# Optimization experiments

Measured on AMD Instinct MI355X. Metric: run time of the kernel, lower is better.

Reference implementation:

```python
import jax, jax.numpy as jnp
import numpy as np
import math

H = 32       # num_attention_heads
HKV = 8      # num_key_value_heads
D = 128      # attention_head_size


def setup_inputs() -> dict:
    key = jax.random.key(0)
    k1, k2, k3 = jax.random.split(key, 3)
    B, L = 2, 2048
    return {
        "query_states": jax.random.normal(k1, (B, L, H * D), dtype=jnp.float32),
        "key_states": jax.random.normal(k2, (B, L, HKV * D), dtype=jnp.float32),
        "value_states": jax.random.normal(k3, (B, L, HKV * D), dtype=jnp.float32),
    }


def reference(query_states, key_states, value_states):
    B, L, _ = query_states.shape
    groups = H // HKV

    # view + transpose(1,2): (B, heads, L, D)
    q = query_states.reshape(B, L, H, D).transpose(0, 2, 1, 3)
    k = key_states.reshape(B, L, HKV, D).transpose(0, 2, 1, 3)
    v = value_states.reshape(B, L, HKV, D).transpose(0, 2, 1, 3)

    # repeat_kv: repeat_interleave along head dim
    k = jnp.repeat(k, groups, axis=1)
    v = jnp.repeat(v, groups, axis=1)

    q = q.astype(jnp.float16)
    k = k.astype(jnp.float16)
    v = v.astype(jnp.float16)

    # source: transpose(1,2) -> (B, L, H, D), then reshape(B*H, L, D)
    # (row-major reshape of the (B,L,H,D) layout, replicated exactly)
    q = q.transpose(0, 2, 1, 3).reshape(B * H, L, D)
    k = k.transpose(0, 2, 1, 3).reshape(B * H, L, D)
    v = v.transpose(0, 2, 1, 3).reshape(B * H, L, D)

    scale = 1.0 / math.sqrt(D)
    attn_scores = jnp.einsum("bqd,bkd->bqk", q, k) * jnp.float16(scale)
    attn_weights = jax.nn.softmax(attn_scores, axis=-1)
    attn_output = jnp.einsum("bqk,bkd->bqd", attn_weights, v)

    # reshape(B,H,L,D).transpose(1,2) -> (B,L,H,D) -> (B, L, H*D)
    attn_output = attn_output.reshape(B, H, L, D).transpose(0, 2, 1, 3)
    return attn_output.reshape(B, L, H * D)
```

## Files before the change

### kernel.cpp

```cpp
#include <hip/hip_runtime.h>

typedef _Float16 f16;
typedef f16 f16x2 __attribute__((ext_vector_type(2)));
typedef f16 f16x4 __attribute__((ext_vector_type(4)));
typedef f16 f16x8 __attribute__((ext_vector_type(8)));
typedef float f32x4 __attribute__((ext_vector_type(4)));

#define NB   2
#define LL   2048
#define LQ   2048
#define LKV  512
#define DD   128
#define BM   128
#define BN   64
#define NKT  (LKV/BN)
#define KS_STR 132
#define VT_STR 68
#define PT_STR 68

#define G_STRIDE 65536ull
#define WS_BYTES (2ull*64ull*G_STRIDE*2ull)

__device__ inline int swz3(int r) { return (r & 3) | ((r & 8) >> 1); }

#define GLOAD16(gsrc, ldst) \
    __builtin_amdgcn_global_load_lds((const __attribute__((address_space(1))) void*)(gsrc), \
                                     (__attribute__((address_space(3))) void*)(ldst), 16, 0, 0)

__global__ __launch_bounds__(256)
void prepack(const float* __restrict__ kg, const float* __restrict__ vg,
             f16* __restrict__ ws)
{
    __shared__ float vtile[64*132];
    const int tid = threadIdx.x;
    const int kt  = blockIdx.x;
    const int g   = blockIdx.y;

    if (blockIdx.z == 0) {
        const float* kb = kg + (size_t)g*65536 + (size_t)kt*8192;
        f16* kout = ws + (size_t)g*G_STRIDE + (size_t)kt*8192;
#pragma unroll
        for (int i = 0; i < 4; ++i) {
            int q = i*256 + tid;
            int r = q >> 4, c = q & 15;
            const float* src = kb + r*128 + ((c ^ swz3(r))*8);
            float4 a = *(const float4*)src;
            float4 b = *(const float4*)(src + 4);
            f16x8 h = { (f16)a.x,(f16)a.y,(f16)a.z,(f16)a.w,
                        (f16)b.x,(f16)b.y,(f16)b.z,(f16)b.w };
            *(f16x8*)(kout + (size_t)q*8) = h;
        }
    } else {
        const float* vb = vg + (size_t)g*65536 + (size_t)kt*8192;
        f16* vout = ws + 64ull*G_STRIDE + (size_t)g*G_STRIDE + (size_t)kt*8192;
#pragma unroll
        for (int i = 0; i < 8; ++i) {
            int f = tid + i*256;
            int row = f >> 5, c4 = f & 31;
            float4 x = *(const float4*)(vb + (size_t)f*4);
            *(float4*)(vtile + row*132 + c4*4) = x;
        }
        __syncthreads();
#pragma unroll
        for (int i = 0; i < 4; ++i) {
            int q = i*256 + tid;
            int r = q >> 3, c = q & 7;
            int kv0 = (c ^ swz3(r))*8;
            f16x8 h;
#pragma unroll
            for (int j = 0; j < 8; ++j) h[j] = (f16)vtile[(kv0+j)*132 + r];
            *(f16x8*)(vout + (size_t)q*8) = h;
        }
    }
}

__global__ __launch_bounds__(256, 3)
void fa_fwd(const float* __restrict__ qg, const f16* __restrict__ ws,
            float* __restrict__ og)
{
    __shared__ __align__(16) f16 Ks[BN*DD];
    __shared__ __align__(16) f16 Vt[DD*BN];

    const int tid  = threadIdx.x;
    const int wave = tid >> 6;
    const int lane = tid & 63;
    const int ln   = lane & 15;
    const int qd   = lane >> 4;

    const int bid = blockIdx.x;
    const int qt  = (bid >> 3) & 15;
    const int g   = ((bid & 7) << 3) | (bid >> 7);
    const int bb  = g >> 5;
    const int lhi = g & 31;

    const float* qmat = qg + (size_t)(bb*LL + 64*lhi)*4096;
    const f16*   kw   = ws + (size_t)g*G_STRIDE;
    const f16*   vw   = ws + (64ull + (size_t)g)*G_STRIDE;

    const int qbase = qt*BM + wave*32;

    auto issueK = [&](int kt) {
#pragma unroll
        for (int i = 0; i < 4; ++i)
            GLOAD16(kw + (size_t)kt*8192 + (size_t)(i*256 + tid)*8,
                    Ks + (i*256 + wave*64)*8);
    };
    auto issueV = [&](int kt) {
#pragma unroll
        for (int i = 0; i < 4; ++i)
            GLOAD16(vw + (size_t)kt*8192 + (size_t)(i*256 + tid)*8,
                    Vt + (i*256 + wave*64)*8);
    };

    issueK(0);
    issueV(0);

    f16x8 qf[2][4];
#pragma unroll
    for (int nt = 0; nt < 2; ++nt) {
        const float* qrow = qmat + (size_t)(qbase + 16*nt + ln)*DD;
#pragma unroll
        for (int kc = 0; kc < 4; ++kc) {
            const float4* qp = (const float4*)(qrow + kc*32 + 8*qd);
            float4 f0 = qp[0], f1 = qp[1];
            f16x8 t = { (f16)f0.x,(f16)f0.y,(f16)f0.z,(f16)f0.w,
                        (f16)f1.x,(f16)f1.y,(f16)f1.z,(f16)f1.w };
            qf[nt][kc] = t;
        }
    }

    f32x4 o[2][8];
#pragma unroll
    for (int nt = 0; nt < 2; ++nt)
#pragma unroll
        for (int dmt = 0; dmt < 8; ++dmt)
#pragma unroll
            for (int r = 0; r < 4; ++r) o[nt][dmt][r] = 0.0f;

    float mrun[2] = {-1e30f, -1e30f}, lrun[2] = {0.0f, 0.0f};
    const float SC2 = 0.08837890625f * 1.44269504088896340f;

    __syncthreads();

#pragma unroll 1
    for (int t = 0; t < NKT; ++t) {
        f32x4 st[2][4];
#pragma unroll
        for (int nt = 0; nt < 2; ++nt)
#pragma unroll
            for (int mt = 0; mt < 4; ++mt)
#pragma unroll
                for (int r = 0; r < 4; ++r) st[nt][mt][r] = 0.0f;
        __builtin_amdgcn_s_setprio(1);
#pragma unroll
        for (int mt = 0; mt < 4; ++mt) {
            const int R = 32*(mt >> 1) + 8*(ln >> 2) + 4*(mt & 1) + (ln & 3);
#pragma unroll
            for (int kc = 0; kc < 4; ++kc) {
                f16x8 af = *(const f16x8*)(Ks + R*DD + (((kc*4 + qd) ^ swz3(R))*8));
#pragma unroll
                for (int nt = 0; nt < 2; ++nt)
                    st[nt][mt] = __builtin_amdgcn_mfma_f32_16x16x32_f16(af, qf[nt][kc], st[nt][mt], 0,0,0);
            }
        }
        __builtin_amdgcn_s_setprio(0);

        float alph[2];
#pragma unroll
        for (int nt = 0; nt < 2; ++nt) {
            float mx = -1e30f;
#pragma unroll
            for (int mt = 0; mt < 4; ++mt)
#pragma unroll
                for (int r = 0; r < 4; ++r) {
                    float v = st[nt][mt][r]*SC2; st[nt][mt][r] = v; mx = fmaxf(mx, v);
                }
            mx = fmaxf(mx, __shfl_xor(mx, 16, 64));
            mx = fmaxf(mx, __shfl_xor(mx, 32, 64));
            float mnew = fmaxf(mrun[nt], mx);
            alph[nt] = exp2f(mrun[nt] - mnew);
            float rs = 0.0f;
#pragma unroll
            for (int mt = 0; mt < 4; ++mt)
#pragma unroll
                for (int r = 0; r < 4; ++r) {
                    float p = exp2f(st[nt][mt][r] - mnew);
                    st[nt][mt][r] = p; rs += p;
                }
            rs += __shfl_xor(rs, 16, 64);
            rs += __shfl_xor(rs, 32, 64);
            lrun[nt] = lrun[nt]*alph[nt] + rs;
            mrun[nt] = mnew;
        }

        __syncthreads();
        if (t+1 < NKT) issueK(t+1);

#pragma unroll
        for (int nt = 0; nt < 2; ++nt)
#pragma unroll
            for (int dmt = 0; dmt < 8; ++dmt)
#pragma unroll
                for (int r = 0; r < 4; ++r) o[nt][dmt][r] *= alph[nt];

#pragma unroll
        for (int kc2 = 0; kc2 < 2; ++kc2) {
            f16x8 pf[2];
#pragma unroll
            for (int nt = 0; nt < 2; ++nt) {
                f16x8 pp = { (f16)st[nt][2*kc2+0][0], (f16)st[nt][2*kc2+0][1],
                             (f16)st[nt][2*kc2+0][2], (f16)st[nt][2*kc2+0][3],
                             (f16)st[nt][2*kc2+1][0], (f16)st[nt][2*kc2+1][1],
                             (f16)st[nt][2*kc2+1][2], (f16)st[nt][2*kc2+1][3] };
                pf[nt] = pp;
            }
            __builtin_amdgcn_s_setprio(1);
#pragma unroll
            for (int dmt = 0; dmt < 8; ++dmt) {
                const int R = 16*dmt + ln;
                f16x8 vf = *(const f16x8*)(Vt + R*BN + (((kc2*4 + qd) ^ swz3(R))*8));
#pragma unroll
                for (int nt = 0; nt < 2; ++nt)
                    o[nt][dmt] = __builtin_amdgcn_mfma_f32_16x16x32_f16(vf, pf[nt], o[nt][dmt], 0,0,0);
            }
            __builtin_amdgcn_s_setprio(0);
        }

        __syncthreads();
        if (t+1 < NKT) issueV(t+1);
    }

#pragma unroll
    for (int nt = 0; nt < 2; ++nt) {
        float inv = 1.0f / lrun[nt];
        int qtok = qbase + 16*nt + ln;
        float* orow = og + (size_t)(bb*LL + qtok)*4096 + lhi*DD + 4*qd;
#pragma unroll
        for (int dmt = 0; dmt < 8; ++dmt) {
            float4 x = { o[nt][dmt][0]*inv, o[nt][dmt][1]*inv,
                         o[nt][dmt][2]*inv, o[nt][dmt][3]*inv };
            *(float4*)(orow + 16*dmt) = x;
        }
    }
}

__global__ __launch_bounds__(256, 2)
void fa_fwd_fb(const float* __restrict__ qg,
               const float* __restrict__ kg,
               const float* __restrict__ vg,
               float* __restrict__ og)
{
    __shared__ __align__(16) f16 smem[BN*KS_STR + DD*VT_STR + BM*PT_STR];
    f16* Ks = smem;
    f16* Vt = smem + BN*KS_STR;
    f16* Pt = smem + BN*KS_STR + DD*VT_STR;

    const int tid  = threadIdx.x;
    const int wave = tid >> 6;
    const int lane = tid & 63;
    const int ln   = lane & 15;
    const int qd   = lane >> 4;

    const int qt   = blockIdx.x;
    const int g    = blockIdx.y;
    const int bb   = g >> 5;
    const int lhi  = g & 31;

    const float* qmat = qg + (size_t)(bb*LL + 64*lhi)*4096;
    const float* kmat = kg + (size_t)(bb*LL + 64*lhi)*1024;
    const float* vmat = vg + (size_t)(bb*LL + 64*lhi)*1024;

    const int qbase = qt*BM + wave*32;

    f16x8 qf[2][4];
#pragma unroll
    for (int nt = 0; nt < 2; ++nt) {
        const float* qrow = qmat + (size_t)(qbase + 16*nt + ln)*DD;
#pragma unroll
        for (int kc = 0; kc < 4; ++kc) {
            const float4* qp = (const float4*)(qrow + kc*32 + 8*qd);
            float4 f0 = qp[0], f1 = qp[1];
            f16x8 t = { (f16)f0.x,(f16)f0.y,(f16)f0.z,(f16)f0.w,
                        (f16)f1.x,(f16)f1.y,(f16)f1.z,(f16)f1.w };
            qf[nt][kc] = t;
        }
    }

    f32x4 o[2][8];
#pragma unroll
    for (int nt = 0; nt < 2; ++nt)
#pragma unroll
        for (int dmt = 0; dmt < 8; ++dmt)
#pragma unroll
            for (int r = 0; r < 4; ++r) o[nt][dmt][r] = 0.0f;

    float mrun[2] = {-1e30f, -1e30f}, lrun[2] = {0.0f, 0.0f};
    const float SC2 = 0.08837890625f * 1.44269504088896340f;

    for (int kt = 0; kt < LKV/BN; ++kt) {
        const float* kb = kmat + kt*BN*DD;
        const float* vb = vmat + kt*BN*DD;

#pragma unroll
        for (int i = 0; i < 8; ++i) {
            int f = tid + i*256;
            int row = f >> 5, c4 = f & 31;
            float4 x = *(const float4*)(kb + f*4);
            f16x4 h4 = { (f16)x.x,(f16)x.y,(f16)x.z,(f16)x.w };
            *(f16x4*)(Ks + row*KS_STR + c4*4) = h4;
        }
#pragma unroll
        for (int i = 0; i < 8; ++i) {
            int f = tid + i*256;
            int kvr = f & 63, c4 = f >> 6;
            float4 x = *(const float4*)(vb + (size_t)kvr*DD + c4*4);
            Vt[(c4*4+0)*VT_STR + kvr] = (f16)x.x;
            Vt[(c4*4+1)*VT_STR + kvr] = (f16)x.y;
            Vt[(c4*4+2)*VT_STR + kvr] = (f16)x.z;
            Vt[(c4*4+3)*VT_STR + kvr] = (f16)x.w;
        }
        __syncthreads();

        f32x4 st[2][4];
#pragma unroll
        for (int nt = 0; nt < 2; ++nt)
#pragma unroll
            for (int mt = 0; mt < 4; ++mt)
#pragma unroll
                for (int r = 0; r < 4; ++r) st[nt][mt][r] = 0.0f;
#pragma unroll
        for (int mt = 0; mt < 4; ++mt) {
            const f16* kr = Ks + (16*mt + ln)*KS_STR + 8*qd;
#pragma unroll
            for (int kc = 0; kc < 4; ++kc) {
                f16x4 a0 = *(const f16x4*)(kr + kc*32);
                f16x4 a1 = *(const f16x4*)(kr + kc*32 + 4);
                f16x8 af = __builtin_shufflevector(a0, a1, 0,1,2,3,4,5,6,7);
#pragma unroll
                for (int nt = 0; nt < 2; ++nt)
                    st[nt][mt] = __builtin_amdgcn_mfma_f32_16x16x32_f16(af, qf[nt][kc], st[nt][mt], 0,0,0);
            }
        }

        float alph[2];
#pragma unroll
        for (int nt = 0; nt < 2; ++nt) {
            float mx = -1e30f;
#pragma unroll
            for (int mt = 0; mt < 4; ++mt)
#pragma unroll
                for (int r = 0; r < 4; ++r) {
                    float v = st[nt][mt][r]*SC2; st[nt][mt][r] = v; mx = fmaxf(mx, v);
                }
            mx = fmaxf(mx, __shfl_xor(mx, 16, 64));
            mx = fmaxf(mx, __shfl_xor(mx, 32, 64));
            float mnew = fmaxf(mrun[nt], mx);
            alph[nt] = exp2f(mrun[nt] - mnew);
            float rs = 0.0f;
#pragma unroll
            for (int mt = 0; mt < 4; ++mt)
#pragma unroll
                for (int r = 0; r < 4; ++r) {
                    float p = exp2f(st[nt][mt][r] - mnew);
                    st[nt][mt][r] = p; rs += p;
                }
            rs += __shfl_xor(rs, 16, 64);
            rs += __shfl_xor(rs, 32, 64);
            lrun[nt] = lrun[nt]*alph[nt] + rs;
            mrun[nt] = mnew;
        }

#pragma unroll
        for (int nt = 0; nt < 2; ++nt) {
            f16* prow = Pt + (wave*32 + 16*nt + ln)*PT_STR + 4*qd;
#pragma unroll
            for (int mt = 0; mt < 4; ++mt)
#pragma unroll
                for (int p2 = 0; p2 < 2; ++p2) {
                    f16x2 pp = { (f16)st[nt][mt][2*p2], (f16)st[nt][mt][2*p2+1] };
                    *(f16x2*)(prow + 16*mt + 2*p2) = pp;
                }
        }

#pragma unroll
        for (int nt = 0; nt < 2; ++nt)
#pragma unroll
            for (int dmt = 0; dmt < 8; ++dmt)
#pragma unroll
                for (int r = 0; r < 4; ++r) o[nt][dmt][r] *= alph[nt];

#pragma unroll
        for (int kc2 = 0; kc2 < 2; ++kc2) {
            f16x8 pf[2];
#pragma unroll
            for (int nt = 0; nt < 2; ++nt) {
                const f16* pr = Pt + (wave*32 + 16*nt + ln)*PT_STR + kc2*32 + 8*qd;
                f16x4 b0 = *(const f16x4*)(pr);
                f16x4 b1 = *(const f16x4*)(pr + 4);
                pf[nt] = __builtin_shufflevector(b0, b1, 0,1,2,3,4,5,6,7);
            }
#pragma unroll
            for (int dmt = 0; dmt < 8; ++dmt) {
                const f16* vr = Vt + (16*dmt + ln)*VT_STR + kc2*32 + 8*qd;
                f16x4 a0 = *(const f16x4*)(vr);
                f16x4 a1 = *(const f16x4*)(vr + 4);
                f16x8 vf = __builtin_shufflevector(a0, a1, 0,1,2,3,4,5,6,7);
#pragma unroll
                for (int nt = 0; nt < 2; ++nt)
                    o[nt][dmt] = __builtin_amdgcn_mfma_f32_16x16x32_f16(vf, pf[nt], o[nt][dmt], 0,0,0);
            }
        }
        __syncthreads();
    }

#pragma unroll
    for (int nt = 0; nt < 2; ++nt) {
        float inv = 1.0f / lrun[nt];
        int qtok = qbase + 16*nt + ln;
        float* orow = og + (size_t)(bb*LL + qtok)*4096 + lhi*DD + 4*qd;
#pragma unroll
        for (int dmt = 0; dmt < 8; ++dmt) {
            float4 x = { o[nt][dmt][0]*inv, o[nt][dmt][1]*inv,
                         o[nt][dmt][2]*inv, o[nt][dmt][3]*inv };
            *(float4*)(orow + 16*dmt) = x;
        }
    }
}

extern "C" void kernel_launch(void* const* d_in, const int* in_sizes, int n_in,
                              void* d_out, int out_size, void* d_ws, size_t ws_size,
                              hipStream_t stream) {
    (void)in_sizes; (void)n_in; (void)out_size;
    const float* q = (const float*)d_in[0];
    const float* k = (const float*)d_in[1];
    const float* v = (const float*)d_in[2];
    float* o = (float*)d_out;
    if (d_ws != nullptr && ws_size >= (size_t)WS_BYTES) {
        hipLaunchKernelGGL(prepack, dim3(8, 64, 2), dim3(256), 0, stream,
                           k, v, (f16*)d_ws);
        hipLaunchKernelGGL(fa_fwd, dim3(1024), dim3(256), 0, stream,
                           q, (const f16*)d_ws, o);
    } else {
        hipLaunchKernelGGL(fa_fwd_fb, dim3(LQ/BM, 64), dim3(256), 0, stream,
                           q, k, v, o);
    }
}
```

Baseline: 202.4 us.

## Double-buffer K/V tiles and skip rescaling when the running max barely changes

Moves K and V shared-memory tiles into two buffers and prefetches the next tile at the top of each iteration, which removes one of the two barriers per iteration and overlaps the loads with compute. The softmax is reworked to fold the scale into an FMA before exp2, and it keeps the old running max (skipping the output rescale) when the new block max exceeds it by no more than 8 in log2 units across the wave. This doubles LDS use to 64KB, which may cut occupancy below the 3-block launch bound. The lazy-rescale threshold lets exponentials reach up to 2^8, so fp16 P values risk precision loss.

After: 238.2 us. 1.18x slower.

```diff
diff --git a/kernel.cpp b/kernel.cpp
--- a/kernel.cpp
+++ b/kernel.cpp
@@ -78,8 +78,8 @@
 void fa_fwd(const float* __restrict__ qg, const f16* __restrict__ ws,
             float* __restrict__ og)
 {
-    __shared__ __align__(16) f16 Ks[BN*DD];
-    __shared__ __align__(16) f16 Vt[DD*BN];
+    __shared__ __align__(16) f16 Ks[2][BN*DD];
+    __shared__ __align__(16) f16 Vt[2][DD*BN];
 
     const int tid  = threadIdx.x;
     const int wave = tid >> 6;
@@ -99,21 +99,21 @@
 
     const int qbase = qt*BM + wave*32;
 
-    auto issueK = [&](int kt) {
+    auto issueK = [&](int kt, int buf) {
 #pragma unroll
         for (int i = 0; i < 4; ++i)
             GLOAD16(kw + (size_t)kt*8192 + (size_t)(i*256 + tid)*8,
-                    Ks + (i*256 + wave*64)*8);
+                    &Ks[buf][(i*256 + wave*64)*8]);
     };
-    auto issueV = [&](int kt) {
+    auto issueV = [&](int kt, int buf) {
 #pragma unroll
         for (int i = 0; i < 4; ++i)
             GLOAD16(vw + (size_t)kt*8192 + (size_t)(i*256 + tid)*8,
-                    Vt + (i*256 + wave*64)*8);
+                    &Vt[buf][(i*256 + wave*64)*8]);
     };
 
-    issueK(0);
-    issueV(0);
+    issueK(0, 0);
+    issueV(0, 0);
 
     f16x8 qf[2][4];
 #pragma unroll
@@ -142,8 +142,11 @@
 
     __syncthreads();
 
+    int cur = 0;
 #pragma unroll 1
     for (int t = 0; t < NKT; ++t) {
+        if (t+1 < NKT) { issueK(t+1, cur^1); issueV(t+1, cur^1); }
+
         f32x4 st[2][4];
 #pragma unroll
         for (int nt = 0; nt < 2; ++nt)
@@ -157,7 +160,7 @@
             const int R = 32*(mt >> 1) + 8*(ln >> 2) + 4*(mt & 1) + (ln & 3);
 #pragma unroll
             for (int kc = 0; kc < 4; ++kc) {
-                f16x8 af = *(const f16x8*)(Ks + R*DD + (((kc*4 + qd) ^ swz3(R))*8));
+                f16x8 af = *(const f16x8*)(&Ks[cur][R*DD + (((kc*4 + qd) ^ swz3(R))*8)]);
 #pragma unroll
                 for (int nt = 0; nt < 2; ++nt)
                     st[nt][mt] = __builtin_amdgcn_mfma_f32_16x16x32_f16(af, qf[nt][kc], st[nt][mt], 0,0,0);
@@ -166,42 +169,50 @@
         __builtin_amdgcn_s_setprio(0);
 
         float alph[2];
+        int skip[2];
 #pragma unroll
         for (int nt = 0; nt < 2; ++nt) {
-            float mx = -1e30f;
-#pragma unroll
-            for (int mt = 0; mt < 4; ++mt)
-#pragma unroll
-                for (int r = 0; r < 4; ++r) {
-                    float v = st[nt][mt][r]*SC2; st[nt][mt][r] = v; mx = fmaxf(mx, v);
-                }
+            float a = fmaxf(fmaxf(st[nt][0][0], st[nt][0][1]), fmaxf(st[nt][0][2], st[nt][0][3]));
+            float b = fmaxf(fmaxf(st[nt][1][0], st[nt][1][1]), fmaxf(st[nt][1][2], st[nt][1][3]));
+            float c = fmaxf(fmaxf(st[nt][2][0], st[nt][2][1]), fmaxf(st[nt][2][2], st[nt][2][3]));
+            float d = fmaxf(fmaxf(st[nt][3][0], st[nt][3][1]), fmaxf(st[nt][3][2], st[nt][3][3]));
+            float mx = fmaxf(fmaxf(a, b), fmaxf(c, d));
             mx = fmaxf(mx, __shfl_xor(mx, 16, 64));
             mx = fmaxf(mx, __shfl_xor(mx, 32, 64));
-            float mnew = fmaxf(mrun[nt], mx);
-            alph[nt] = exp2f(mrun[nt] - mnew);
-            float rs = 0.0f;
-#pragma unroll
-            for (int mt = 0; mt < 4; ++mt)
-#pragma unroll
-                for (int r = 0; r < 4; ++r) {
-                    float p = exp2f(st[nt][mt][r] - mnew);
-                    st[nt][mt][r] = p; rs += p;
-                }
+            float mxs = mx * SC2;
+            int s = __all(mxs - mrun[nt] <= 8.0f);
+            if (s) {
+                alph[nt] = 1.0f;
+            } else {
+                float mnew = fmaxf(mrun[nt], mxs);
+                alph[nt] = exp2f(mrun[nt] - mnew);
+                mrun[nt] = mnew;
+            }
+            skip[nt] = s;
+            const float mm = mrun[nt];
+#pragma unroll
+            for (int mt = 0; mt < 4; ++mt)
+#pragma unroll
+                for (int r = 0; r < 4; ++r)
+                    st[nt][mt][r] = exp2f(__builtin_fmaf(st[nt][mt][r], SC2, -mm));
+            float s0 = (st[nt][0][0] + st[nt][0][1]) + (st[nt][0][2] + st[nt][0][3]);
+            float s1 = (st[nt][1][0] + st[nt][1][1]) + (st[nt][1][2] + st[nt][1][3]);
+            float s2 = (st[nt][2][0] + st[nt][2][1]) + (st[nt][2][2] + st[nt][2][3]);
+            float s3 = (st[nt][3][0] + st[nt][3][1]) + (st[nt][3][2] + st[nt][3][3]);
+            float rs = (s0 + s1) + (s2 + s3);
             rs += __shfl_xor(rs, 16, 64);
             rs += __shfl_xor(rs, 32, 64);
-            lrun[nt] = lrun[nt]*alph[nt] + rs;
-            mrun[nt] = mnew;
-        }
-
-        __syncthreads();
-        if (t+1 < NKT) issueK(t+1);
-
-#pragma unroll
-        for (int nt = 0; nt < 2; ++nt)
-#pragma unroll
-            for (int dmt = 0; dmt < 8; ++dmt)
-#pragma unroll
-                for (int r = 0; r < 4; ++r) o[nt][dmt][r] *= alph[nt];
+            lrun[nt] = __builtin_fmaf(lrun[nt], alph[nt], rs);
+        }
+
+        if (!(skip[0] & skip[1])) {
+#pragma unroll
+            for (int nt = 0; nt < 2; ++nt)
+#pragma unroll
+                for (int dmt = 0; dmt < 8; ++dmt)
+#pragma unroll
+                    for (int r = 0; r < 4; ++r) o[nt][dmt][r] *= alph[nt];
+        }
 
 #pragma unroll
         for (int kc2 = 0; kc2 < 2; ++kc2) {
@@ -218,7 +229,7 @@
 #pragma unroll
             for (int dmt = 0; dmt < 8; ++dmt) {
                 const int R = 16*dmt + ln;
-                f16x8 vf = *(const f16x8*)(Vt + R*BN + (((kc2*4 + qd) ^ swz3(R))*8));
+                f16x8 vf = *(const f16x8*)(&Vt[cur][R*BN + (((kc2*4 + qd) ^ swz3(R))*8)]);
 #pragma unroll
                 for (int nt = 0; nt < 2; ++nt)
                     o[nt][dmt] = __builtin_amdgcn_mfma_f32_16x16x32_f16(vf, pf[nt], o[nt][dmt], 0,0,0);
@@ -226,8 +237,7 @@
             __builtin_amdgcn_s_setprio(0);
         }
 
-        __syncthreads();
-        if (t+1 < NKT) issueV(t+1);
+        if (t+1 < NKT) { __syncthreads(); cur ^= 1; }
     }
 
 #pragma unroll
```
